# Performance work log

Hardware: AMD Instinct MI355X
Metric: run time of the kernel (lower is better)

Reference implementation:

```python
import jax, jax.numpy as jnp
import numpy as np

NUM_HEADS = 12  # per init_kwargs


def setup_inputs() -> dict:
    key = jax.random.key(0)
    k1, k2, k3 = jax.random.split(key, 3)
    B, H, W, D = 1, 64, 64, 768
    x = jax.random.normal(k1, (B, H, W, D), dtype=jnp.float32)
    # torch nn.Linear weights are [out, in]; small init keeps softmax well-conditioned
    w_qkv = jax.random.normal(k2, (3 * D, D), dtype=jnp.float32) * 0.02
    w_proj = jax.random.normal(k3, (D, D), dtype=jnp.float32) * 0.02
    b_proj = jnp.zeros((D,), dtype=jnp.float32)
    return {"x": x, "w_qkv": w_qkv, "w_proj": w_proj, "b_proj": b_proj}


def reference(x, w_qkv, w_proj, b_proj):
    B, H, W, D = x.shape
    S = H * W
    nh = NUM_HEADS
    hd = D // nh
    scale = hd ** (-0.5)
    # qkv: [B, S, 3, nh, hd] -> q,k,v each [B, nh, S, hd]
    qkv = jnp.einsum('bhwd,ed->bhwe', x, w_qkv).reshape(B, S, 3, nh, hd)
    qkv = jnp.transpose(qkv, (2, 0, 3, 1, 4))
    q, k, v = qkv[0], qkv[1], qkv[2]
    # full O(S^2) attention matrix, as in the original module
    wei = jnp.einsum('bnqd,bnkd->bnqk', q * scale, k)
    wei = jax.nn.softmax(wei, axis=-1)
    # att_drop omitted (eval mode / deterministic baseline)
    out = jnp.einsum('bnqk,bnkd->bnqd', wei, v)  # [B, nh, S, hd]
    # [B, nh, H, W, hd] -> [B, H, W, nh*hd]
    out = jnp.transpose(out.reshape(B, nh, H, W, hd), (0, 2, 3, 1, 4)).reshape(B, H, W, D)
    proj = jnp.einsum('bhwd,ed->bhwe', out, w_proj) + b_proj
    return proj
```

## Files before the change

kernel.cpp:

```cpp
#include <hip/hip_runtime.h>
#include <hip/hip_bf16.h>

typedef short s16x8 __attribute__((ext_vector_type(8)));
typedef float f32x4 __attribute__((ext_vector_type(4)));
typedef __hip_bfloat16 bf16;

#define GLD16(g, l)                                                        \
  __builtin_amdgcn_global_load_lds(                                        \
      (const __attribute__((address_space(1))) void*)(g),                  \
      (__attribute__((address_space(3))) void*)(l), 16, 0, 0)

#define MFMA16(a, b, c) __builtin_amdgcn_mfma_f32_16x16x32_bf16((a), (b), (c), 0, 0, 0)

static constexpr int kS = 4096;
static constexpr int kD = 768;
static constexpr int kNH = 12;
static constexpr int kHD = 64;
static constexpr int kNE = 2304;

__global__ __launch_bounds__(256)
void k_cvt(const float* __restrict__ src, bf16* __restrict__ dst, int n8) {
  const int i = blockIdx.x * blockDim.x + threadIdx.x;
  if (i >= n8) return;
  const f32x4 a = *(const f32x4*)(src + i * 8);
  const f32x4 b = *(const f32x4*)(src + i * 8 + 4);
  s16x8 o;
#pragma unroll
  for (int j = 0; j < 4; ++j) {
    o[j] = (short)__bfloat16_as_ushort(__float2bfloat16(a[j]));
    o[j + 4] = (short)__bfloat16_as_ushort(__float2bfloat16(b[j]));
  }
  *(s16x8*)((short*)dst + i * 8) = o;
}

__global__ __launch_bounds__(256, 2)
void k_qkv(const bf16* __restrict__ X, const bf16* __restrict__ W,
           bf16* __restrict__ Qw, bf16* __restrict__ Kw, bf16* __restrict__ Vw) {
  __shared__ __align__(16) short As[128 * 32];
  __shared__ __align__(16) short Bs[128 * 32];
  const int tid = threadIdx.x;
  const int wv = tid >> 6, ln = tid & 63;
  const int r = ln & 15, kq = ln >> 4;
  const int bm = blockIdx.x * 128;
  const int bn = blockIdx.y * 128;
  const int wr = wv >> 1, wc = wv & 1;
  const short* Xs = (const short*)X;
  const short* Ws = (const short*)W;

  f32x4 acc[4][4] = {};

  const int c0 = wv * 128 + ln, c1 = c0 + 64;
  const int ra0 = c0 >> 2, ka0 = c0 & 3;
  const int ra1 = c1 >> 2, ka1 = c1 & 3;
  short* aDst0 = As + wv * 1024; short* aDst1 = aDst0 + 512;
  short* bDst0 = Bs + wv * 1024; short* bDst1 = bDst0 + 512;
  const short* gA0 = Xs + (bm + ra0) * kD + ka0 * 8;
  const short* gA1 = Xs + (bm + ra1) * kD + ka1 * 8;
  const short* gB0 = Ws + (bn + ra0) * kD + ka0 * 8;
  const short* gB1 = Ws + (bn + ra1) * kD + ka1 * 8;

  for (int k0 = 0; k0 < kD; k0 += 32) {
    GLD16(gA0 + k0, aDst0);
    GLD16(gA1 + k0, aDst1);
    GLD16(gB0 + k0, bDst0);
    GLD16(gB1 + k0, bDst1);
    __syncthreads();
    s16x8 a[4], b[4];
#pragma unroll
    for (int i = 0; i < 4; ++i)
      a[i] = *(const s16x8*)(As + (wr * 64 + i * 16 + r) * 32 + kq * 8);
#pragma unroll
    for (int j = 0; j < 4; ++j)
      b[j] = *(const s16x8*)(Bs + (wc * 64 + j * 16 + r) * 32 + kq * 8);
#pragma unroll
    for (int i = 0; i < 4; ++i)
#pragma unroll
      for (int j = 0; j < 4; ++j) acc[i][j] = MFMA16(a[i], b[j], acc[i][j]);
    __syncthreads();
  }

  const int which = bn / kD;
  bf16* dst = (which == 0) ? Qw : (which == 1) ? Kw : Vw;
  const float scl = (which == 0) ? 0.125f : 1.0f;
  const int ebase = bn - which * kD + wc * 64;
#pragma unroll
  for (int j = 0; j < 4; ++j) {
    const int e = ebase + j * 16 + r;
    const int h = e >> 6, d = e & 63;
#pragma unroll
    for (int i = 0; i < 4; ++i) {
      const int srow = bm + wr * 64 + i * 16 + kq * 4;
#pragma unroll
      for (int rr = 0; rr < 4; ++rr)
        dst[(h * kS + srow + rr) * kHD + d] = __float2bfloat16(acc[i][j][rr] * scl);
    }
  }
}

__global__ __launch_bounds__(256, 2)
void k_vt(const bf16* __restrict__ Vw, bf16* __restrict__ Vt) {
  __shared__ __align__(16) short L[64 * 72];
  const int h = blockIdx.y, st = blockIdx.x;
  const int t = threadIdx.x;
  const short* src = (const short*)Vw + (h * kS + st * 64) * kHD;
  short* dstb = (short*)Vt + h * kHD * kS;
#pragma unroll
  for (int u = 0; u < 2; ++u) {
    const int c = u * 256 + t;
    const int row = c >> 3, ch = c & 7;
    *(s16x8*)(L + row * 72 + ch * 8) = *(const s16x8*)(src + row * kHD + ch * 8);
  }
  __syncthreads();
#pragma unroll
  for (int u = 0; u < 2; ++u) {
    const int c = u * 256 + t;
    const int d = c >> 3, ch = c & 7;
    s16x8 v;
#pragma unroll
    for (int j = 0; j < 8; ++j) v[j] = L[(ch * 8 + j) * 72 + d];
    *(s16x8*)(dstb + d * kS + st * 64 + ch * 8) = v;
  }
}

__global__ __launch_bounds__(256, 2)
void k_attn(const bf16* __restrict__ Qw, const bf16* __restrict__ Kw,
            const bf16* __restrict__ Vt, bf16* __restrict__ Att) {
  __shared__ __align__(16) short Ks[64 * 64];
  __shared__ __align__(16) short Vs[64 * 64];
  __shared__ __align__(16) bf16 Ps[4][16][72];
  const int tid = threadIdx.x;
  const int wv = tid >> 6, ln = tid & 63;
  const int r = ln & 15, kq = ln >> 4;
  const int h = blockIdx.y;
  const int q0 = blockIdx.x * 64;
  const short* Qh = (const short*)Qw + (h * kS + q0) * kHD;
  const short* Kh = (const short*)Kw + h * kS * kHD;
  const short* Vh = (const short*)Vt + h * kHD * kS;

  s16x8 aq[2];
#pragma unroll
  for (int ks = 0; ks < 2; ++ks)
    aq[ks] = *(const s16x8*)(Qh + (wv * 16 + r) * kHD + ks * 32 + kq * 8);

  f32x4 o[4] = {};
  float lp[4] = {0.f, 0.f, 0.f, 0.f};

  const int c0 = wv * 128 + ln, c1 = c0 + 64;
  const int kr0 = c0 >> 3, g0 = (c0 & 7) ^ (kr0 & 7);
  const int kr1 = c1 >> 3, g1 = (c1 & 7) ^ (kr1 & 7);
  short* kDst0 = Ks + wv * 1024; short* kDst1 = kDst0 + 512;
  short* vDst0 = Vs + wv * 1024; short* vDst1 = vDst0 + 512;

  for (int kt = 0; kt < kS / 64; ++kt) {
    GLD16(Kh + (kt * 64 + kr0) * kHD + g0 * 8, kDst0);
    GLD16(Kh + (kt * 64 + kr1) * kHD + g1 * 8, kDst1);
    GLD16(Vh + kr0 * kS + kt * 64 + g0 * 8, vDst0);
    GLD16(Vh + kr1 * kS + kt * 64 + g1 * 8, vDst1);
    __syncthreads();

    f32x4 sf[4];
#pragma unroll
    for (int nt = 0; nt < 4; ++nt) {
      const int R = nt * 16 + r;
      const int sw = R & 7;
      s16x8 b0 = *(const s16x8*)(Ks + R * 64 + ((kq) ^ sw) * 8);
      s16x8 b1 = *(const s16x8*)(Ks + R * 64 + ((kq + 4) ^ sw) * 8);
      f32x4 z = {};
      z = MFMA16(aq[0], b0, z);
      z = MFMA16(aq[1], b1, z);
      sf[nt] = z;
    }

#pragma unroll
    for (int nt = 0; nt < 4; ++nt) {
#pragma unroll
      for (int rr = 0; rr < 4; ++rr) {
        const float p = __expf(sf[nt][rr]);
        lp[rr] += p;
        Ps[wv][kq * 4 + rr][nt * 16 + r] = __float2bfloat16(p);
      }
    }
    asm volatile("s_waitcnt lgkmcnt(0)" ::: "memory");

    s16x8 pa0 = *(const s16x8*)&Ps[wv][r][kq * 8];
    s16x8 pa1 = *(const s16x8*)&Ps[wv][r][32 + kq * 8];
#pragma unroll
    for (int nt = 0; nt < 4; ++nt) {
      const int R = nt * 16 + r;
      const int sw = R & 7;
      s16x8 v0 = *(const s16x8*)(Vs + R * 64 + ((kq) ^ sw) * 8);
      s16x8 v1 = *(const s16x8*)(Vs + R * 64 + ((kq + 4) ^ sw) * 8);
      o[nt] = MFMA16(pa0, v0, o[nt]);
      o[nt] = MFMA16(pa1, v1, o[nt]);
    }
    __syncthreads();
  }

  float inv[4];
#pragma unroll
  for (int rr = 0; rr < 4; ++rr) {
    float v = lp[rr];
    v += __shfl_xor(v, 1);
    v += __shfl_xor(v, 2);
    v += __shfl_xor(v, 4);
    v += __shfl_xor(v, 8);
    inv[rr] = 1.0f / v;
  }
#pragma unroll
  for (int nt = 0; nt < 4; ++nt) {
    const int d = nt * 16 + r;
#pragma unroll
    for (int rr = 0; rr < 4; ++rr) {
      const int srow = q0 + wv * 16 + kq * 4 + rr;
      Att[srow * kD + h * kHD + d] = __float2bfloat16(o[nt][rr] * inv[rr]);
    }
  }
}

__global__ __launch_bounds__(256, 2)
void k_proj(const bf16* __restrict__ A, const bf16* __restrict__ W,
            const float* __restrict__ Bias, float* __restrict__ Out) {
  __shared__ __align__(16) short As[128 * 32];
  __shared__ __align__(16) short Bs[128 * 32];
  const int tid = threadIdx.x;
  const int wv = tid >> 6, ln = tid & 63;
  const int r = ln & 15, kq = ln >> 4;
  const int bm = blockIdx.x * 128;
  const int bn = blockIdx.y * 128;
  const int wr = wv >> 1, wc = wv & 1;
  const short* Asrc = (const short*)A;
  const short* Wsrc = (const short*)W;

  f32x4 acc[4][4] = {};
  const int c0 = wv * 128 + ln, c1 = c0 + 64;
  const int ra0 = c0 >> 2, ka0 = c0 & 3;
  const int ra1 = c1 >> 2, ka1 = c1 & 3;
  short* aDst0 = As + wv * 1024; short* aDst1 = aDst0 + 512;
  short* bDst0 = Bs + wv * 1024; short* bDst1 = bDst0 + 512;
  const short* gA0 = Asrc + (bm + ra0) * kD + ka0 * 8;
  const short* gA1 = Asrc + (bm + ra1) * kD + ka1 * 8;
  const short* gB0 = Wsrc + (bn + ra0) * kD + ka0 * 8;
  const short* gB1 = Wsrc + (bn + ra1) * kD + ka1 * 8;

  for (int k0 = 0; k0 < kD; k0 += 32) {
    GLD16(gA0 + k0, aDst0);
    GLD16(gA1 + k0, aDst1);
    GLD16(gB0 + k0, bDst0);
    GLD16(gB1 + k0, bDst1);
    __syncthreads();
    s16x8 a[4], b[4];
#pragma unroll
    for (int i = 0; i < 4; ++i)
      a[i] = *(const s16x8*)(As + (wr * 64 + i * 16 + r) * 32 + kq * 8);
#pragma unroll
    for (int j = 0; j < 4; ++j)
      b[j] = *(const s16x8*)(Bs + (wc * 64 + j * 16 + r) * 32 + kq * 8);
#pragma unroll
    for (int i = 0; i < 4; ++i)
#pragma unroll
      for (int j = 0; j < 4; ++j) acc[i][j] = MFMA16(a[i], b[j], acc[i][j]);
    __syncthreads();
  }
#pragma unroll
  for (int j = 0; j < 4; ++j) {
    const int e = bn + wc * 64 + j * 16 + r;
    const float bv = Bias[e];
#pragma unroll
    for (int i = 0; i < 4; ++i) {
      const int srow = bm + wr * 64 + i * 16 + kq * 4;
#pragma unroll
      for (int rr = 0; rr < 4; ++rr)
        Out[(srow + rr) * kD + e] = acc[i][j][rr] + bv;
    }
  }
}

extern "C" void kernel_launch(void* const* d_in, const int* in_sizes, int n_in,
                              void* d_out, int out_size, void* d_ws, size_t ws_size,
                              hipStream_t stream) {
  const float* x = (const float*)d_in[0];
  const float* w_qkv = (const float*)d_in[1];
  const float* w_proj = (const float*)d_in[2];
  const float* b_proj = (const float*)d_in[3];
  float* out = (float*)d_out;

  const size_t HS = (size_t)kNH * kS * kHD;
  const int nX = kS * kD;
  const int nWq = kNE * kD;
  const int nWp = kD * kD;

  bf16* Xb = (bf16*)d_ws;
  bf16* Wqb = Xb + nX;
  bf16* Wpb = Wqb + nWq;
  bf16* Qw = Wpb + nWp;
  bf16* Kw = Qw + HS;
  bf16* Vw = Kw + HS;
  bf16* Vt = Vw + HS;
  bf16* At = Vt + HS;

  k_cvt<<<(nX / 8 + 255) / 256, 256, 0, stream>>>(x, Xb, nX / 8);
  k_cvt<<<(nWq / 8 + 255) / 256, 256, 0, stream>>>(w_qkv, Wqb, nWq / 8);
  k_cvt<<<(nWp / 8 + 255) / 256, 256, 0, stream>>>(w_proj, Wpb, nWp / 8);

  k_qkv<<<dim3(kS / 128, kNE / 128), 256, 0, stream>>>(Xb, Wqb, Qw, Kw, Vw);
  k_vt<<<dim3(kS / 64, kNH), 256, 0, stream>>>(Vw, Vt);
  k_attn<<<dim3(kS / 64, kNH), 256, 0, stream>>>(Qw, Kw, Vt, At);
  k_proj<<<dim3(kS / 128, kD / 128), 256, 0, stream>>>(At, Wpb, b_proj, out);
}
```

Before: 146.6 us.

## Double-buffer GEMM and attention tiles, fuse conversions, use exp2, shrink proj tiles

Merges the three fp32-to-bf16 conversion launches into one kernel. Adds LDS double buffering with prefetch of the next K-tile in the QKV GEMM, the attention loop and the projection GEMM, cutting one barrier per iteration. Folds log2(e) into the Q scale so softmax can use exp2f, and adds s_setprio around the MFMA phases. The projection now uses 64x64 tiles for more blocks, and occupancy hints are raised to 3. Double buffering grows LDS use, which may limit occupancy. Reusing a buffer before every wave has finished reading it could race, since the loop keeps only the end-of-iteration barrier.

```diff
diff --git a/kernel.cpp b/kernel.cpp
--- a/kernel.cpp
+++ b/kernel.cpp
@@ -1,5 +1,6 @@
 #include <hip/hip_runtime.h>
 #include <hip/hip_bf16.h>
+#include <math.h>
 
 typedef short s16x8 __attribute__((ext_vector_type(8)));
 typedef float f32x4 __attribute__((ext_vector_type(4)));
@@ -18,10 +19,25 @@
 static constexpr int kHD = 64;
 static constexpr int kNE = 2304;
 
+static constexpr int kNX8 = kS * kD / 8;
+static constexpr int kNWq8 = kNE * kD / 8;
+static constexpr int kNWp8 = kD * kD / 8;
+
 __global__ __launch_bounds__(256)
-void k_cvt(const float* __restrict__ src, bf16* __restrict__ dst, int n8) {
-  const int i = blockIdx.x * blockDim.x + threadIdx.x;
-  if (i >= n8) return;
+void k_cvt3(const float* __restrict__ x, const float* __restrict__ wq,
+            const float* __restrict__ wp, bf16* __restrict__ xb,
+            bf16* __restrict__ wqb, bf16* __restrict__ wpb) {
+  int i = blockIdx.x * 256 + threadIdx.x;
+  const float* src;
+  short* dst;
+  if (i < kNX8) {
+    src = x; dst = (short*)xb;
+  } else if (i < kNX8 + kNWq8) {
+    i -= kNX8; src = wq; dst = (short*)wqb;
+  } else {
+    i -= kNX8 + kNWq8; if (i >= kNWp8) return;
+    src = wp; dst = (short*)wpb;
+  }
   const f32x4 a = *(const f32x4*)(src + i * 8);
   const f32x4 b = *(const f32x4*)(src + i * 8 + 4);
   s16x8 o;
@@ -30,14 +46,14 @@
     o[j] = (short)__bfloat16_as_ushort(__float2bfloat16(a[j]));
     o[j + 4] = (short)__bfloat16_as_ushort(__float2bfloat16(b[j]));
   }
-  *(s16x8*)((short*)dst + i * 8) = o;
+  *(s16x8*)(dst + i * 8) = o;
 }
 
 __global__ __launch_bounds__(256, 2)
 void k_qkv(const bf16* __restrict__ X, const bf16* __restrict__ W,
            bf16* __restrict__ Qw, bf16* __restrict__ Kw, bf16* __restrict__ Vw) {
-  __shared__ __align__(16) short As[128 * 32];
-  __shared__ __align__(16) short Bs[128 * 32];
+  __shared__ __align__(16) short As[2][128 * 32];
+  __shared__ __align__(16) short Bs[2][128 * 32];
   const int tid = threadIdx.x;
   const int wv = tid >> 6, ln = tid & 63;
   const int r = ln & 15, kq = ln >> 4;
@@ -52,26 +68,38 @@
   const int c0 = wv * 128 + ln, c1 = c0 + 64;
   const int ra0 = c0 >> 2, ka0 = c0 & 3;
   const int ra1 = c1 >> 2, ka1 = c1 & 3;
-  short* aDst0 = As + wv * 1024; short* aDst1 = aDst0 + 512;
-  short* bDst0 = Bs + wv * 1024; short* bDst1 = bDst0 + 512;
+  const int off0 = wv * 1024, off1 = off0 + 512;
   const short* gA0 = Xs + (bm + ra0) * kD + ka0 * 8;
   const short* gA1 = Xs + (bm + ra1) * kD + ka1 * 8;
   const short* gB0 = Ws + (bn + ra0) * kD + ka0 * 8;
   const short* gB1 = Ws + (bn + ra1) * kD + ka1 * 8;
 
-  for (int k0 = 0; k0 < kD; k0 += 32) {
-    GLD16(gA0 + k0, aDst0);
-    GLD16(gA1 + k0, aDst1);
-    GLD16(gB0 + k0, bDst0);
-    GLD16(gB1 + k0, bDst1);
-    __syncthreads();
+  GLD16(gA0, &As[0][off0]);
+  GLD16(gA1, &As[0][off1]);
+  GLD16(gB0, &Bs[0][off0]);
+  GLD16(gB1, &Bs[0][off1]);
+  __syncthreads();
+
+  const int NT = kD / 32;
+  for (int t = 0; t < NT; ++t) {
+    const short* aCur = As[t & 1];
+    const short* bCur = Bs[t & 1];
+    if (t + 1 < NT) {
+      const int k1 = (t + 1) * 32;
+      short* aN = As[(t + 1) & 1];
+      short* bN = Bs[(t + 1) & 1];
+      GLD16(gA0 + k1, aN + off0);
+      GLD16(gA1 + k1, aN + off1);
+      GLD16(gB0 + k1, bN + off0);
+      GLD16(gB1 + k1, bN + off1);
+    }
     s16x8 a[4], b[4];
 #pragma unroll
     for (int i = 0; i < 4; ++i)
-      a[i] = *(const s16x8*)(As + (wr * 64 + i * 16 + r) * 32 + kq * 8);
+      a[i] = *(const s16x8*)(aCur + (wr * 64 + i * 16 + r) * 32 + kq * 8);
 #pragma unroll
     for (int j = 0; j < 4; ++j)
-      b[j] = *(const s16x8*)(Bs + (wc * 64 + j * 16 + r) * 32 + kq * 8);
+      b[j] = *(const s16x8*)(bCur + (wc * 64 + j * 16 + r) * 32 + kq * 8);
 #pragma unroll
     for (int i = 0; i < 4; ++i)
 #pragma unroll
@@ -81,7 +109,7 @@
 
   const int which = bn / kD;
   bf16* dst = (which == 0) ? Qw : (which == 1) ? Kw : Vw;
-  const float scl = (which == 0) ? 0.125f : 1.0f;
+  const float scl = (which == 0) ? 0.125f * 1.44269504088896f : 1.0f;
   const int ebase = bn - which * kD + wc * 64;
 #pragma unroll
   for (int j = 0; j < 4; ++j) {
@@ -122,11 +150,11 @@
   }
 }
 
-__global__ __launch_bounds__(256, 2)
+__global__ __launch_bounds__(256, 3)
 void k_attn(const bf16* __restrict__ Qw, const bf16* __restrict__ Kw,
             const bf16* __restrict__ Vt, bf16* __restrict__ Att) {
-  __shared__ __align__(16) short Ks[64 * 64];
-  __shared__ __align__(16) short Vs[64 * 64];
+  __shared__ __align__(16) short Ks[2][64 * 64];
+  __shared__ __align__(16) short Vs[2][64 * 64];
   __shared__ __align__(16) bf16 Ps[4][16][72];
   const int tid = threadIdx.x;
   const int wv = tid >> 6, ln = tid & 63;
@@ -148,34 +176,53 @@
   const int c0 = wv * 128 + ln, c1 = c0 + 64;
   const int kr0 = c0 >> 3, g0 = (c0 & 7) ^ (kr0 & 7);
   const int kr1 = c1 >> 3, g1 = (c1 & 7) ^ (kr1 & 7);
-  short* kDst0 = Ks + wv * 1024; short* kDst1 = kDst0 + 512;
-  short* vDst0 = Vs + wv * 1024; short* vDst1 = vDst0 + 512;
-
-  for (int kt = 0; kt < kS / 64; ++kt) {
-    GLD16(Kh + (kt * 64 + kr0) * kHD + g0 * 8, kDst0);
-    GLD16(Kh + (kt * 64 + kr1) * kHD + g1 * 8, kDst1);
-    GLD16(Vh + kr0 * kS + kt * 64 + g0 * 8, vDst0);
-    GLD16(Vh + kr1 * kS + kt * 64 + g1 * 8, vDst1);
-    __syncthreads();
+  const int off0 = wv * 1024, off1 = off0 + 512;
+  const short* gK0 = Kh + kr0 * kHD + g0 * 8;
+  const short* gK1 = Kh + kr1 * kHD + g1 * 8;
+  const short* gV0 = Vh + kr0 * kS + g0 * 8;
+  const short* gV1 = Vh + kr1 * kS + g1 * 8;
+
+  GLD16(gK0, &Ks[0][off0]);
+  GLD16(gK1, &Ks[0][off1]);
+  GLD16(gV0, &Vs[0][off0]);
+  GLD16(gV1, &Vs[0][off1]);
+  __syncthreads();
+
+  const int NT = kS / 64;
+  for (int kt = 0; kt < NT; ++kt) {
+    const short* ksCur = Ks[kt & 1];
+    const short* vsCur = Vs[kt & 1];
+    if (kt + 1 < NT) {
+      short* ksN = Ks[(kt + 1) & 1];
+      short* vsN = Vs[(kt + 1) & 1];
+      const int dk = (kt + 1) * 64 * kHD;
+      const int dv = (kt + 1) * 64;
+      GLD16(gK0 + dk, ksN + off0);
+      GLD16(gK1 + dk, ksN + off1);
+      GLD16(gV0 + dv, vsN + off0);
+      GLD16(gV1 + dv, vsN + off1);
+    }
 
     f32x4 sf[4];
+    __builtin_amdgcn_s_setprio(1);
 #pragma unroll
     for (int nt = 0; nt < 4; ++nt) {
       const int R = nt * 16 + r;
       const int sw = R & 7;
-      s16x8 b0 = *(const s16x8*)(Ks + R * 64 + ((kq) ^ sw) * 8);
-      s16x8 b1 = *(const s16x8*)(Ks + R * 64 + ((kq + 4) ^ sw) * 8);
+      s16x8 b0 = *(const s16x8*)(ksCur + R * 64 + ((kq) ^ sw) * 8);
+      s16x8 b1 = *(const s16x8*)(ksCur + R * 64 + ((kq + 4) ^ sw) * 8);
       f32x4 z = {};
       z = MFMA16(aq[0], b0, z);
       z = MFMA16(aq[1], b1, z);
       sf[nt] = z;
     }
+    __builtin_amdgcn_s_setprio(0);
 
 #pragma unroll
     for (int nt = 0; nt < 4; ++nt) {
 #pragma unroll
       for (int rr = 0; rr < 4; ++rr) {
-        const float p = __expf(sf[nt][rr]);
+        const float p = exp2f(sf[nt][rr]);
         lp[rr] += p;
         Ps[wv][kq * 4 + rr][nt * 16 + r] = __float2bfloat16(p);
       }
@@ -184,15 +231,17 @@
 
     s16x8 pa0 = *(const s16x8*)&Ps[wv][r][kq * 8];
     s16x8 pa1 = *(const s16x8*)&Ps[wv][r][32 + kq * 8];
+    __builtin_amdgcn_s_setprio(1);
 #pragma unroll
     for (int nt = 0; nt < 4; ++nt) {
       const int R = nt * 16 + r;
       const int sw = R & 7;
-      s16x8 v0 = *(const s16x8*)(Vs + R * 64 + ((kq) ^ sw) * 8);
-      s16x8 v1 = *(const s16x8*)(Vs + R * 64 + ((kq + 4) ^ sw) * 8);
+      s16x8 v0 = *(const s16x8*)(vsCur + R * 64 + ((kq) ^ sw) * 8);
+      s16x8 v1 = *(const s16x8*)(vsCur + R * 64 + ((kq + 4) ^ sw) * 8);
       o[nt] = MFMA16(pa0, v0, o[nt]);
       o[nt] = MFMA16(pa1, v1, o[nt]);
     }
+    __builtin_amdgcn_s_setprio(0);
     __syncthreads();
   }
 
@@ -217,57 +266,60 @@
   }
 }
 
-__global__ __launch_bounds__(256, 2)
+__global__ __launch_bounds__(256, 3)
 void k_proj(const bf16* __restrict__ A, const bf16* __restrict__ W,
             const float* __restrict__ Bias, float* __restrict__ Out) {
-  __shared__ __align__(16) short As[128 * 32];
-  __shared__ __align__(16) short Bs[128 * 32];
+  __shared__ __align__(16) short As[2][64 * 32];
+  __shared__ __align__(16) short Bs[2][64 * 32];
   const int tid = threadIdx.x;
   const int wv = tid >> 6, ln = tid & 63;
   const int r = ln & 15, kq = ln >> 4;
-  const int bm = blockIdx.x * 128;
-  const int bn = blockIdx.y * 128;
+  const int bm = blockIdx.x * 64;
+  const int bn = blockIdx.y * 64;
   const int wr = wv >> 1, wc = wv & 1;
   const short* Asrc = (const short*)A;
   const short* Wsrc = (const short*)W;
 
-  f32x4 acc[4][4] = {};
-  const int c0 = wv * 128 + ln, c1 = c0 + 64;
-  const int ra0 = c0 >> 2, ka0 = c0 & 3;
-  const int ra1 = c1 >> 2, ka1 = c1 & 3;
-  short* aDst0 = As + wv * 1024; short* aDst1 = aDst0 + 512;
-  short* bDst0 = Bs + wv * 1024; short* bDst1 = bDst0 + 512;
-  const short* gA0 = Asrc + (bm + ra0) * kD + ka0 * 8;
-  const short* gA1 = Asrc + (bm + ra1) * kD + ka1 * 8;
-  const short* gB0 = Wsrc + (bn + ra0) * kD + ka0 * 8;
-  const short* gB1 = Wsrc + (bn + ra1) * kD + ka1 * 8;
-
-  for (int k0 = 0; k0 < kD; k0 += 32) {
-    GLD16(gA0 + k0, aDst0);
-    GLD16(gA1 + k0, aDst1);
-    GLD16(gB0 + k0, bDst0);
-    GLD16(gB1 + k0, bDst1);
+  f32x4 acc[2][2] = {};
+  const int c = wv * 64 + ln;
+  const int ra = c >> 2, ka = c & 3;
+  const int off = wv * 512;
+  const short* gA = Asrc + (bm + ra) * kD + ka * 8;
+  const short* gB = Wsrc + (bn + ra) * kD + ka * 8;
+
+  GLD16(gA, &As[0][off]);
+  GLD16(gB, &Bs[0][off]);
+  __syncthreads();
+
+  const int NT = kD / 32;
+  for (int t = 0; t < NT; ++t) {
+    const short* aCur = As[t & 1];
+    const short* bCur = Bs[t & 1];
+    if (t + 1 < NT) {
+      const int k1 = (t + 1) * 32;
+      GLD16(gA + k1, &As[(t + 1) & 1][off]);
+      GLD16(gB + k1, &Bs[(t + 1) & 1][off]);
+    }
+    s16x8 a[2], b[2];
+#pragma unroll
+    for (int i = 0; i < 2; ++i)
+      a[i] = *(const s16x8*)(aCur + (wr * 32 + i * 16 + r) * 32 + kq * 8);
+#pragma unroll
+    for (int j = 0; j < 2; ++j)
+      b[j] = *(const s16x8*)(bCur + (wc * 32 + j * 16 + r) * 32 + kq * 8);
+#pragma unroll
+    for (int i = 0; i < 2; ++i)
+#pragma unroll
+      for (int j = 0; j < 2; ++j) acc[i][j] = MFMA16(a[i], b[j], acc[i][j]);
     __syncthreads();
-    s16x8 a[4], b[4];
-#pragma unroll
-    for (int i = 0; i < 4; ++i)
-      a[i] = *(const s16x8*)(As + (wr * 64 + i * 16 + r) * 32 + kq * 8);
-#pragma unroll
-    for (int j = 0; j < 4; ++j)
-      b[j] = *(const s16x8*)(Bs + (wc * 64 + j * 16 + r) * 32 + kq * 8);
-#pragma unroll
-    for (int i = 0; i < 4; ++i)
-#pragma unroll
-      for (int j = 0; j < 4; ++j) acc[i][j] = MFMA16(a[i], b[j], acc[i][j]);
-    __syncthreads();
-  }
-#pragma unroll
-  for (int j = 0; j < 4; ++j) {
-    const int e = bn + wc * 64 + j * 16 + r;
+  }
+#pragma unroll
+  for (int j = 0; j < 2; ++j) {
+    const int e = bn + wc * 32 + j * 16 + r;
     const float bv = Bias[e];
 #pragma unroll
-    for (int i = 0; i < 4; ++i) {
-      const int srow = bm + wr * 64 + i * 16 + kq * 4;
+    for (int i = 0; i < 2; ++i) {
+      const int srow = bm + wr * 32 + i * 16 + kq * 4;
 #pragma unroll
       for (int rr = 0; rr < 4; ++rr)
         Out[(srow + rr) * kD + e] = acc[i][j][rr] + bv;
@@ -298,12 +350,11 @@
   bf16* Vt = Vw + HS;
   bf16* At = Vt + HS;
 
-  k_cvt<<<(nX / 8 + 255) / 256, 256, 0, stream>>>(x, Xb, nX / 8);
-  k_cvt<<<(nWq / 8 + 255) / 256, 256, 0, stream>>>(w_qkv, Wqb, nWq / 8);
-  k_cvt<<<(nWp / 8 + 255) / 256, 256, 0, stream>>>(w_proj, Wpb, nWp / 8);
+  const int totalC = kNX8 + kNWq8 + kNWp8;
+  k_cvt3<<<(totalC + 255) / 256, 256, 0, stream>>>(x, w_qkv, w_proj, Xb, Wqb, Wpb);
 
   k_qkv<<<dim3(kS / 128, kNE / 128), 256, 0, stream>>>(Xb, Wqb, Qw, Kw, Vw);
   k_vt<<<dim3(kS / 64, kNH), 256, 0, stream>>>(Vw, Vt);
   k_attn<<<dim3(kS / 64, kNH), 256, 0, stream>>>(Qw, Kw, Vt, At);
-  k_proj<<<dim3(kS / 128, kD / 128), 256, 0, stream>>>(At, Wpb, b_proj, out);
-}
+  k_proj<<<dim3(kS / 64, kD / 64), 256, 0, stream>>>(At, Wpb, b_proj, out);
+}
```

After: 158.4 us. 1.08x slower.
